# Kernel optimization log

Measured on AMD Instinct MI355X. Metric: run time of the kernel, lower is better.

The kernel has to match this reference:

```python
import jax, jax.numpy as jnp
import numpy as np
import math

EPS = 1e-6
TEMPERATURE = 1.0
NEG = -100.0


def setup_inputs() -> dict:
    key = jax.random.key(0)
    k1, k2, k3 = jax.random.split(key, 3)
    B, N, C = 16, 2048, 64
    x = jax.random.normal(k1, (B, N, C), dtype=jnp.float32)
    y = jax.random.normal(k2, (B, N, C), dtype=jnp.float32)
    # complementary keep / pruned gates, as produced by the TPS token scorer
    keep = jax.random.bernoulli(k3, 0.5, (B, N, 1)).astype(jnp.float32)
    pruned = 1.0 - keep
    return {
        "x": x,
        "y": y,
        "current_keep_decision": keep,
        "current_pruned_decision": pruned,
    }


def reference(x, y, current_keep_decision, current_pruned_decision):
    # Training branch of TPSModule.forward (module defaults to training mode).
    B, N, C = x.shape
    # --- get_sim(x, None, mask_eye=-100, l2_norm=True) ---
    xn = x / (jnp.linalg.norm(x, axis=-1, keepdims=True) + EPS)
    sim = jnp.einsum("bnc,bmc->bnm", xn, xn)  # [B, N, N]
    eye = jnp.eye(N, dtype=bool)
    sim = jnp.where(eye[None, :, :], NEG, sim)
    sim = sim / TEMPERATURE
    # mask out columns of non-kept tokens
    keep_b = current_keep_decision.reshape(B, 1, N).astype(bool)
    sim = jnp.where(keep_b, sim, NEG)
    # hard top-1 (with ties) per row, gated by pruned flag of the source row
    sim_th = jnp.max(sim, axis=2, keepdims=True)  # [B, N, 1]
    mask = (sim == sim_th).astype(x.dtype) * current_pruned_decision  # [B, N, N]
    cos = mask * sim
    # transpose: now rows index destination (kept) tokens
    mask_t = mask.transpose(0, 2, 1)
    cos_t = cos.transpose(0, 2, 1)
    numerator = jnp.exp(cos_t) * mask_t  # [B, N, N]
    denominator = math.e + jnp.sum(numerator, axis=-1, keepdims=True)  # [B, N, 1]
    out = x * (math.e / denominator) + jnp.einsum(
        "bnm,bmc->bnc", numerator / denominator, x
    )
    return out
```

## Files before the change

### kernel.cpp

```cpp
#include <hip/hip_runtime.h>
#include <math.h>

#define BB 16
#define NN 2048
#define CC 64
#define TPB 256
#define MROWS 16
#define RPW 4
#define E_CONST 2.71828182845904523536f

__global__ __launch_bounds__(TPB) void k_pre(const float* __restrict__ keep,
                                             float* __restrict__ outz,
                                             float* __restrict__ S,
                                             int* __restrict__ cntP,
                                             int* __restrict__ cntK,
                                             int* __restrict__ listP,
                                             int* __restrict__ listK) {
    const int tid = threadIdx.x, lane = tid & 63;

    float4* o4 = (float4*)outz + (size_t)blockIdx.x * 1024;
    float4 z = {0.0f, 0.0f, 0.0f, 0.0f};
#pragma unroll
    for (int i = 0; i < 4; ++i) o4[i * TPB + tid] = z;

    const int b = blockIdx.x;
    if (b >= BB) return;

    __shared__ int cP, cK;
    if (tid == 0) { cP = 0; cK = 0; }
    __syncthreads();
    for (int i = tid; i < NN; i += TPB) S[b * NN + i] = 0.0f;
    const unsigned long long lt = (lane == 63) ? 0x7fffffffffffffffull
                                               : ((1ull << lane) - 1ull);
#pragma unroll
    for (int it = 0; it < NN / TPB; ++it) {
        int n = it * TPB + tid;
        bool kp = keep[b * NN + n] != 0.0f;
        unsigned long long mk = __ballot(kp);
        int nk = __popcll(mk);
        int bk = 0, bp = 0;
        if (lane == 0) {
            bk = atomicAdd(&cK, nk);
            bp = atomicAdd(&cP, 64 - nk);
        }
        bk = __shfl(bk, 0); bp = __shfl(bp, 0);
        int pk = __popcll(mk & lt);
        if (kp) listK[b * NN + bk + pk] = n;
        else    listP[b * NN + bp + (lane - pk)] = n;
    }
    __syncthreads();
    if (tid == 0) { cntP[b] = cP; cntK[b] = cK; }
}

__global__ __launch_bounds__(TPB) void k_pre2(const float* __restrict__ x,
                                              const int* __restrict__ cntK,
                                              const int* __restrict__ listK,
                                              float4* __restrict__ colM) {
    const int b = blockIdx.y;
    const int colp = blockIdx.x * TPB + threadIdx.x;
    const int K = cntK[b];
    bool ok = colp < K;
    int tok = ok ? listK[b * NN + colp] : 0;
    const float4* x4 = (const float4*)(x + (size_t)b * NN * CC);
    float4 v[16];
    float sq = 0.0f;
#pragma unroll
    for (int k4 = 0; k4 < 16; ++k4) {
        v[k4] = x4[(size_t)tok * 16 + k4];
        sq += v[k4].x * v[k4].x + v[k4].y * v[k4].y
            + v[k4].z * v[k4].z + v[k4].w * v[k4].w;
    }
    float iv = ok ? 1.0f / (sqrtf(sq) + 1e-6f) : 0.0f;
#pragma unroll
    for (int k4 = 0; k4 < 16; ++k4) {
        float4 w = v[k4];
        w.x *= iv; w.y *= iv; w.z *= iv; w.w *= iv;
        colM[((size_t)b * 16 + k4) * NN + colp] = w;
    }
}

__global__ __launch_bounds__(TPB, 4) void k_argmax(
    const float* __restrict__ x,
    const float4* __restrict__ colM,
    const int*   __restrict__ cntP,
    const int*   __restrict__ cntK,
    const int*   __restrict__ listP,
    const int*   __restrict__ listK,
    float* __restrict__ S,
    float* __restrict__ A) {

    const int b    = blockIdx.x & 15;
    const int tile = blockIdx.x >> 4;
    const int P = cntP[b], K = cntK[b];
    const int base = tile * MROWS;
    if (base >= P) return;

    const int tid = threadIdx.x;
    const int wid = tid >> 6;
    const int lane = tid & 63;

    int rtok[RPW];
#pragma unroll
    for (int r = 0; r < RPW; ++r) {
        int rid = base + wid * RPW + r;
        int tok = (rid < P) ? listP[b * NN + rid] : 0;
        rtok[r] = __builtin_amdgcn_readfirstlane(tok);
    }
    const float4* x4 = (const float4*)(x + (size_t)b * NN * CC);
    const float4* cm = colM + (size_t)b * 16 * NN;

    float    tmax[RPW];
    unsigned msk[RPW];
#pragma unroll
    for (int r = 0; r < RPW; ++r) { tmax[r] = -3.0e38f; msk[r] = 0u; }

    const int ntiles = (K + 511) >> 9;

    for (int t = 0; t < ntiles; ++t) {
        const int cstart = t * 512;

        float acc[RPW][8];
#pragma unroll
        for (int r = 0; r < RPW; ++r)
#pragma unroll
            for (int j = 0; j < 8; ++j) acc[r][j] = 0.0f;

#pragma unroll 2
        for (int k4 = 0; k4 < 16; ++k4) {
            float4 rv[RPW];
#pragma unroll
            for (int r = 0; r < RPW; ++r)
                rv[r] = x4[(size_t)rtok[r] * 16 + k4];
            const float4* cmk = cm + (size_t)k4 * NN + cstart + lane;
            float4 cv[8];
#pragma unroll
            for (int j = 0; j < 8; ++j)
                cv[j] = cmk[j * 64];
#pragma unroll
            for (int r = 0; r < RPW; ++r)
#pragma unroll
                for (int j = 0; j < 8; ++j)
                    acc[r][j] = fmaf(rv[r].x, cv[j].x,
                                fmaf(rv[r].y, cv[j].y,
                                fmaf(rv[r].z, cv[j].z,
                                fmaf(rv[r].w, cv[j].w, acc[r][j]))));
        }

#pragma unroll
        for (int r = 0; r < RPW; ++r)
#pragma unroll
            for (int j = 0; j < 8; ++j) {
                int colp = cstart + j * 64 + lane;
                float s = (colp < K) ? acc[r][j] : -1.0e30f;
                unsigned bit = 1u << ((t << 3) | j);
                if (s > tmax[r])       { tmax[r] = s; msk[r] = bit; }
                else if (s == tmax[r])  msk[r] |= bit;
            }
    }

    int nvr = P - base - wid * RPW;
    for (int r = 0; r < RPW; ++r) {
        if (r >= nvr) break;
        float m = tmax[r];
#pragma unroll
        for (int off = 32; off; off >>= 1) m = fmaxf(m, __shfl_xor(m, off, 64));
        int src = rtok[r];
        float xv = x[(size_t)(b * NN + src) * CC + lane];
        float sq = xv * xv;
#pragma unroll
        for (int off = 32; off; off >>= 1) sq += __shfl_xor(sq, off, 64);
        float ivr = 1.0f / (sqrtf(sq) + 1e-6f);
        float wgt = expf(m * ivr);
        unsigned long long bal = __ballot(tmax[r] == m && msk[r] != 0u);
        while (bal) {
            int sl = __ffsll(bal) - 1;
            bal &= bal - 1;
            unsigned mm = __shfl(msk[r], sl);
            while (mm) {
                int bit = __ffs(mm) - 1;
                mm &= mm - 1;
                int colp = ((bit >> 3) * 512) + ((bit & 7) * 64) + sl;
                int dst = listK[b * NN + colp];
                atomicAdd(&A[(size_t)(b * NN + dst) * CC + lane], wgt * xv);
                if (lane == 0) atomicAdd(&S[b * NN + dst], wgt);
            }
        }
    }
}

__global__ __launch_bounds__(TPB) void k_finalize(const float* __restrict__ x,
                                                  const float* __restrict__ S,
                                                  float* __restrict__ out) {
    int i = blockIdx.x * TPB + threadIdx.x;
    int row = i >> 4;
    float inv = 1.0f / (E_CONST + S[row]);
    float4 xv = ((const float4*)x)[i];
    float4 av = ((float4*)out)[i];
    float4 o;
    o.x = (xv.x * E_CONST + av.x) * inv;
    o.y = (xv.y * E_CONST + av.y) * inv;
    o.z = (xv.z * E_CONST + av.z) * inv;
    o.w = (xv.w * E_CONST + av.w) * inv;
    ((float4*)out)[i] = o;
}

extern "C" void kernel_launch(void* const* d_in, const int* in_sizes, int n_in,
                              void* d_out, int out_size, void* d_ws, size_t ws_size,
                              hipStream_t stream) {
    const float* x    = (const float*)d_in[0];
    const float* keep = (const float*)d_in[2];
    float* out = (float*)d_out;

    char* ws = (char*)d_ws;
    float* S    = (float*)(ws + (128 << 10));
    int*   cntP = (int*)(ws + (256 << 10));
    int*   cntK = cntP + 16;
    int*   listP = (int*)(ws + (256 << 10) + 128);
    int*   listK = listP + BB * NN;
    float4* colM = (float4*)(ws + (1 << 20));

    k_pre<<<512, TPB, 0, stream>>>(keep, out, S, cntP, cntK, listP, listK);

    dim3 gp2(NN / TPB, BB);
    k_pre2<<<gp2, TPB, 0, stream>>>(x, cntK, listK, colM);

    k_argmax<<<(NN / MROWS) * BB, TPB, 0, stream>>>(x, colM, cntP, cntK,
                                                    listP, listK, S, out);

    k_finalize<<<(BB * NN * CC / 4) / TPB, TPB, 0, stream>>>(x, S, out);
}
```

Measured before the change: 147.5 us.

## Trim argmax column tiles to K and make normalization wave-per-token

k_argmax no longer always processes 512-column tiles. The last tile is sized to the remaining kept columns (512, 256 or 128), which cuts wasted FMAs on padded columns, and the tie mask becomes a 64-bit per-64-column-block bitmap. k_pre2 now uses one wave per kept token with coalesced reads and a shuffle reduction, instead of one thread per token loading 64 floats. It also zero-fills up to 128 columns past K so the smaller tiles read defined data. The cost is extra code paths, more template instantiations and added register pressure.

```diff
diff --git a/kernel.cpp b/kernel.cpp
--- a/kernel.cpp
+++ b/kernel.cpp
@@ -55,28 +55,76 @@
 __global__ __launch_bounds__(TPB) void k_pre2(const float* __restrict__ x,
                                               const int* __restrict__ cntK,
                                               const int* __restrict__ listK,
-                                              float4* __restrict__ colM) {
-    const int b = blockIdx.y;
-    const int colp = blockIdx.x * TPB + threadIdx.x;
-    const int K = cntK[b];
-    bool ok = colp < K;
-    int tok = ok ? listK[b * NN + colp] : 0;
-    const float4* x4 = (const float4*)(x + (size_t)b * NN * CC);
-    float4 v[16];
-    float sq = 0.0f;
-#pragma unroll
+                                              float* __restrict__ colMf) {
+    const int b    = blockIdx.x & 15;
+    const int seg  = blockIdx.x >> 4;
+    const int lane = threadIdx.x & 63;
+    const int wid  = threadIdx.x >> 6;
+    const int wave = seg * 4 + wid;
+    const int K    = cntK[b];
+    const int Kend = min(NN, K + 128);
+
+    const float* xb = x + (size_t)b * NN * CC;
+    float* cf = colMf + (size_t)b * 16 * NN * 4;
+
+    for (int colp = wave; colp < Kend; colp += 256) {
+        float v = 0.0f;
+        if (colp < K) {
+            int tok = listK[b * NN + colp];
+            float xv = xb[(size_t)tok * CC + lane];
+            float sq = xv * xv;
+#pragma unroll
+            for (int off = 32; off; off >>= 1) sq += __shfl_xor(sq, off, 64);
+            v = xv / (sqrtf(sq) + 1e-6f);
+        }
+        cf[((size_t)(lane >> 2) * NN + colp) * 4 + (lane & 3)] = v;
+    }
+}
+
+template <int J>
+__device__ __forceinline__ void tile_body(const float4* __restrict__ x4,
+                                          const float4* __restrict__ cm,
+                                          const int* rtok, int cstart, int K,
+                                          int lane, float* tmax,
+                                          unsigned long long* msk) {
+    float acc[RPW][J];
+#pragma unroll
+    for (int r = 0; r < RPW; ++r)
+#pragma unroll
+        for (int j = 0; j < J; ++j) acc[r][j] = 0.0f;
+
+#pragma unroll 2
     for (int k4 = 0; k4 < 16; ++k4) {
-        v[k4] = x4[(size_t)tok * 16 + k4];
-        sq += v[k4].x * v[k4].x + v[k4].y * v[k4].y
-            + v[k4].z * v[k4].z + v[k4].w * v[k4].w;
-    }
-    float iv = ok ? 1.0f / (sqrtf(sq) + 1e-6f) : 0.0f;
-#pragma unroll
-    for (int k4 = 0; k4 < 16; ++k4) {
-        float4 w = v[k4];
-        w.x *= iv; w.y *= iv; w.z *= iv; w.w *= iv;
-        colM[((size_t)b * 16 + k4) * NN + colp] = w;
-    }
+        float4 rv[RPW];
+#pragma unroll
+        for (int r = 0; r < RPW; ++r)
+            rv[r] = x4[(size_t)rtok[r] * 16 + k4];
+        const float4* cmk = cm + (size_t)k4 * NN + cstart + lane;
+        float4 cv[J];
+#pragma unroll
+        for (int j = 0; j < J; ++j)
+            cv[j] = cmk[j * 64];
+#pragma unroll
+        for (int r = 0; r < RPW; ++r)
+#pragma unroll
+            for (int j = 0; j < J; ++j)
+                acc[r][j] = fmaf(rv[r].x, cv[j].x,
+                            fmaf(rv[r].y, cv[j].y,
+                            fmaf(rv[r].z, cv[j].z,
+                            fmaf(rv[r].w, cv[j].w, acc[r][j]))));
+    }
+
+    const int cb0 = cstart >> 6;
+#pragma unroll
+    for (int r = 0; r < RPW; ++r)
+#pragma unroll
+        for (int j = 0; j < J; ++j) {
+            int colp = cstart + j * 64 + lane;
+            float s = (colp < K) ? acc[r][j] : -1.0e30f;
+            unsigned long long bit = 1ull << (cb0 + j);
+            if (s > tmax[r])       { tmax[r] = s; msk[r] = bit; }
+            else if (s == tmax[r])  msk[r] |= bit;
+        }
 }
 
 __global__ __launch_bounds__(TPB, 4) void k_argmax(
@@ -109,53 +157,24 @@
     const float4* x4 = (const float4*)(x + (size_t)b * NN * CC);
     const float4* cm = colM + (size_t)b * 16 * NN;
 
-    float    tmax[RPW];
-    unsigned msk[RPW];
-#pragma unroll
-    for (int r = 0; r < RPW; ++r) { tmax[r] = -3.0e38f; msk[r] = 0u; }
-
-    const int ntiles = (K + 511) >> 9;
-
-    for (int t = 0; t < ntiles; ++t) {
-        const int cstart = t * 512;
-
-        float acc[RPW][8];
-#pragma unroll
-        for (int r = 0; r < RPW; ++r)
-#pragma unroll
-            for (int j = 0; j < 8; ++j) acc[r][j] = 0.0f;
-
-#pragma unroll 2
-        for (int k4 = 0; k4 < 16; ++k4) {
-            float4 rv[RPW];
-#pragma unroll
-            for (int r = 0; r < RPW; ++r)
-                rv[r] = x4[(size_t)rtok[r] * 16 + k4];
-            const float4* cmk = cm + (size_t)k4 * NN + cstart + lane;
-            float4 cv[8];
-#pragma unroll
-            for (int j = 0; j < 8; ++j)
-                cv[j] = cmk[j * 64];
-#pragma unroll
-            for (int r = 0; r < RPW; ++r)
-#pragma unroll
-                for (int j = 0; j < 8; ++j)
-                    acc[r][j] = fmaf(rv[r].x, cv[j].x,
-                                fmaf(rv[r].y, cv[j].y,
-                                fmaf(rv[r].z, cv[j].z,
-                                fmaf(rv[r].w, cv[j].w, acc[r][j]))));
-        }
-
-#pragma unroll
-        for (int r = 0; r < RPW; ++r)
-#pragma unroll
-            for (int j = 0; j < 8; ++j) {
-                int colp = cstart + j * 64 + lane;
-                float s = (colp < K) ? acc[r][j] : -1.0e30f;
-                unsigned bit = 1u << ((t << 3) | j);
-                if (s > tmax[r])       { tmax[r] = s; msk[r] = bit; }
-                else if (s == tmax[r])  msk[r] |= bit;
-            }
+    float              tmax[RPW];
+    unsigned long long msk[RPW];
+#pragma unroll
+    for (int r = 0; r < RPW; ++r) { tmax[r] = -3.0e38f; msk[r] = 0ull; }
+
+    int cstart = 0;
+    while (cstart < K) {
+        int rem = K - cstart;
+        if (rem > 384) {
+            tile_body<8>(x4, cm, rtok, cstart, K, lane, tmax, msk);
+            cstart += 512;
+        } else if (rem > 128) {
+            tile_body<4>(x4, cm, rtok, cstart, K, lane, tmax, msk);
+            cstart += 256;
+        } else {
+            tile_body<2>(x4, cm, rtok, cstart, K, lane, tmax, msk);
+            cstart += 128;
+        }
     }
 
     int nvr = P - base - wid * RPW;
@@ -171,15 +190,15 @@
         for (int off = 32; off; off >>= 1) sq += __shfl_xor(sq, off, 64);
         float ivr = 1.0f / (sqrtf(sq) + 1e-6f);
         float wgt = expf(m * ivr);
-        unsigned long long bal = __ballot(tmax[r] == m && msk[r] != 0u);
+        unsigned long long bal = __ballot(tmax[r] == m && msk[r] != 0ull);
         while (bal) {
             int sl = __ffsll(bal) - 1;
             bal &= bal - 1;
-            unsigned mm = __shfl(msk[r], sl);
+            unsigned long long mm = __shfl(msk[r], sl);
             while (mm) {
-                int bit = __ffs(mm) - 1;
+                int cb = __ffsll(mm) - 1;
                 mm &= mm - 1;
-                int colp = ((bit >> 3) * 512) + ((bit & 7) * 64) + sl;
+                int colp = (cb << 6) + sl;
                 int dst = listK[b * NN + colp];
                 atomicAdd(&A[(size_t)(b * NN + dst) * CC + lane], wgt * xv);
                 if (lane == 0) atomicAdd(&S[b * NN + dst], wgt);
@@ -217,15 +236,15 @@
     int*   cntK = cntP + 16;
     int*   listP = (int*)(ws + (256 << 10) + 128);
     int*   listK = listP + BB * NN;
-    float4* colM = (float4*)(ws + (1 << 20));
+    float* colMf = (float*)(ws + (1 << 20));
 
     k_pre<<<512, TPB, 0, stream>>>(keep, out, S, cntP, cntK, listP, listK);
 
-    dim3 gp2(NN / TPB, BB);
-    k_pre2<<<gp2, TPB, 0, stream>>>(x, cntK, listK, colM);
-
-    k_argmax<<<(NN / MROWS) * BB, TPB, 0, stream>>>(x, colM, cntP, cntK,
-                                                    listP, listK, S, out);
+    k_pre2<<<BB * 64, TPB, 0, stream>>>(x, cntK, listK, colMf);
+
+    k_argmax<<<(NN / MROWS) * BB, TPB, 0, stream>>>(x, (const float4*)colMf,
+                                                    cntP, cntK, listP, listK,
+                                                    S, out);
 
     k_finalize<<<(BB * NN * CC / 4) / TPB, TPB, 0, stream>>>(x, S, out);
 }
```

Result: faster. 140.6 us (-4.6%).
